# Optimization experiments

Hardware: AMD Instinct MI355X
Metric: run time of the kernel (lower is better)

Reference implementation:

```python
import jax, jax.numpy as jnp
import numpy as np
import math

B, S, D = 4, 2048, 1024
H, DH = 16, 64  # num_heads, head dim (hardcoded 64 in module)


def setup_inputs() -> dict:
    key = jax.random.key(0)
    ks = jax.random.split(key, 5)
    scale = 0.02
    return {
        "x": jax.random.normal(ks[0], (B, S, D), dtype=jnp.float32),
        "W_Q": jax.random.normal(ks[1], (D, H * DH), dtype=jnp.float32) * scale,
        "W_K": jax.random.normal(ks[2], (D, H * DH), dtype=jnp.float32) * scale,
        "W_V": jax.random.normal(ks[3], (D, H * DH), dtype=jnp.float32) * scale,
        "W_O": jax.random.normal(ks[4], (H * DH, D), dtype=jnp.float32) * scale,
        "ln_gamma": jnp.ones((D,), dtype=jnp.float32),
        "ln_beta": jnp.zeros((D,), dtype=jnp.float32),
    }


def reference(x, W_Q, W_K, W_V, W_O, ln_gamma, ln_beta):
    # QKV projections (bias=False Linear: x @ W)
    q = (x @ W_Q).reshape(B, S, H, DH).transpose(0, 2, 1, 3)  # [B,H,S,DH]
    k = (x @ W_K).reshape(B, S, H, DH).transpose(0, 2, 1, 3)
    v = (x @ W_V).reshape(B, S, H, DH).transpose(0, 2, 1, 3)

    # scaled scores with causal mask (upper triangle, diag=1 -> -1e7)
    scores = jnp.einsum("bhsd,bhtd->bhst", q, k) / math.sqrt(DH)  # [B,H,S,S]
    causal = jnp.triu(jnp.ones((S, S), dtype=bool), k=1)
    scores = jnp.where(causal, jnp.float32(-1e7), scores)
    attn = jax.nn.softmax(scores, axis=-1)
    ctx = jnp.einsum("bhst,bhtd->bhsd", attn, v)  # [B,H,S,DH]

    # merge heads, output proj, residual, LayerNorm
    out = ctx.transpose(0, 2, 1, 3).reshape(B, S, H * DH) @ W_O + x
    mu = jnp.mean(out, axis=-1, keepdims=True)
    var = jnp.mean((out - mu) ** 2, axis=-1, keepdims=True)
    out = (out - mu) * jax.lax.rsqrt(var + 1e-5) * ln_gamma + ln_beta
    return out
```

## Files before the change

### kernel.cpp

```cpp
#include <hip/hip_runtime.h>
#include <hip/hip_bf16.h>
#include <cstdint>
#include <cstddef>

#define S_ 2048
#define D_ 1024
#define H_ 16
#define DH_ 64
#define M_ 8192

using bf16 = __bf16;
using bf16x4 = __attribute__((ext_vector_type(4))) __bf16;
using bf16x8 = __attribute__((ext_vector_type(8))) __bf16;
using f32x4 = __attribute__((ext_vector_type(4))) float;
using s16x4 = __attribute__((ext_vector_type(4))) short;

__device__ __forceinline__ void g2lds16(const bf16* g, bf16* l) {
  __builtin_amdgcn_global_load_lds(
      (const __attribute__((address_space(1))) void*)g,
      (__attribute__((address_space(3))) void*)l, 16, 0, 0);
}

__device__ __forceinline__ f32x4 mfma16(bf16x4 a, bf16x4 b, f32x4 c) {
#if __has_builtin(__builtin_amdgcn_mfma_f32_16x16x16_bf16)
  return __builtin_amdgcn_mfma_f32_16x16x16_bf16(a, b, c, 0, 0, 0);
#elif __has_builtin(__builtin_amdgcn_mfma_f32_16x16x16bf16_1k)
  return __builtin_amdgcn_mfma_f32_16x16x16bf16_1k(
      __builtin_bit_cast(s16x4, a), __builtin_bit_cast(s16x4, b), c, 0, 0, 0);
#else
  f32x4 d;
  asm("v_mfma_f32_16x16x16_bf16 %0, %1, %2, %3"
      : "=v"(d)
      : "v"(a), "v"(b), "v"(c));
  return d;
#endif
}

__global__ __launch_bounds__(256) void cvt_all_kernel(
    const float* __restrict__ x, const float* __restrict__ w0,
    const float* __restrict__ w1, const float* __restrict__ w2,
    const float* __restrict__ w3, bf16* __restrict__ xb,
    bf16* __restrict__ o0, bf16* __restrict__ o1, bf16* __restrict__ o2,
    bf16* __restrict__ o3) {
  __shared__ float tile[32][33];
  int bx = blockIdx.x;
  int tid = threadIdx.x;
  if (bx < 4096) {
    size_t i = ((size_t)bx * 256 + tid) * 8;
    float4 a = *(const float4*)(x + i);
    float4 b = *(const float4*)(x + i + 4);
    bf16x8 o;
    o[0] = (bf16)a.x; o[1] = (bf16)a.y; o[2] = (bf16)a.z; o[3] = (bf16)a.w;
    o[4] = (bf16)b.x; o[5] = (bf16)b.y; o[6] = (bf16)b.z; o[7] = (bf16)b.w;
    *(bf16x8*)(xb + i) = o;
    return;
  }
  int wb = bx - 4096;
  int wsel = wb >> 10; wb &= 1023;
  const float* W; bf16* O;
  switch (wsel) {
    case 0: W = w0; O = o0; break;
    case 1: W = w1; O = o1; break;
    case 2: W = w2; O = o2; break;
    default: W = w3; O = o3; break;
  }
  int n0 = (wb & 31) * 32;
  int k0 = (wb >> 5) * 32;
#pragma unroll
  for (int i = 0; i < 4; ++i) {
    int e = tid + i * 256; int rr = e >> 5, cc = e & 31;
    tile[rr][cc] = W[(size_t)(k0 + rr) * 1024 + n0 + cc];
  }
  __syncthreads();
#pragma unroll
  for (int i = 0; i < 4; ++i) {
    int e = tid + i * 256; int rr = e >> 5, cc = e & 31;
    O[(size_t)(n0 + rr) * 1024 + k0 + cc] = (bf16)tile[cc][rr];
  }
}

template <int MODE>
__global__ __launch_bounds__(256) void gemm_kernel(
    const bf16* __restrict__ A,
    const bf16* __restrict__ Bt0, const bf16* __restrict__ Bt1,
    const bf16* __restrict__ Bt2,
    bf16* __restrict__ Qo, bf16* __restrict__ Ko, bf16* __restrict__ Vto,
    const float* __restrict__ xres, float* __restrict__ out) {
  __shared__ __align__(16) bf16 smA[128 * 32];
  __shared__ __align__(16) bf16 smB[128 * 32];
  constexpr int NBLK = (MODE == 0) ? 24 : 8;
  int bm = blockIdx.x / NBLK, bn = blockIdx.x % NBLK;
  int m0 = bm * 128;
  const bf16* Bt; int which = 0, n0;
  if constexpr (MODE == 0) {
    which = bn >> 3; n0 = (bn & 7) * 128;
    Bt = (which == 0) ? Bt0 : (which == 1 ? Bt1 : Bt2);
  } else { n0 = bn * 128; Bt = Bt0; }

  int tid = threadIdx.x;
  int wave = tid >> 6, lane = tid & 63;
  int quad = lane >> 4, r = lane & 15;
  int wm = (wave >> 1) * 64, wn = (wave & 1) * 64;

  f32x4 acc[4][4];
  f32x4 zero = {0.f, 0.f, 0.f, 0.f};
#pragma unroll
  for (int i = 0; i < 4; ++i)
#pragma unroll
    for (int j = 0; j < 4; ++j) acc[i][j] = zero;

  int c0 = 2 * wave, c1 = 2 * wave + 1;
  int rA0 = c0 * 16 + (lane >> 2);
  int rA1 = c1 * 16 + (lane >> 2);
  int kc = (lane & 3) * 8;

  for (int k0 = 0; k0 < 1024; k0 += 32) {
    __syncthreads();
    const bf16 *gA0, *gA1;
    if constexpr (MODE == 0) {
      gA0 = A + (size_t)(m0 + rA0) * 1024 + k0 + kc;
      gA1 = A + (size_t)(m0 + rA1) * 1024 + k0 + kc;
    } else {
      int kk = k0 + kc, h = kk >> 6, dh = kk & 63;
      int mm0 = m0 + rA0, mm1 = m0 + rA1;
      gA0 = A + ((size_t)((mm0 >> 11) * H_ + h) * S_ + (mm0 & 2047)) * DH_ + dh;
      gA1 = A + ((size_t)((mm1 >> 11) * H_ + h) * S_ + (mm1 & 2047)) * DH_ + dh;
    }
    g2lds16(gA0, smA + c0 * 512);
    g2lds16(gA1, smA + c1 * 512);
    g2lds16(Bt + (size_t)(n0 + rA0) * 1024 + k0 + kc, smB + c0 * 512);
    g2lds16(Bt + (size_t)(n0 + rA1) * 1024 + k0 + kc, smB + c1 * 512);
    __syncthreads();
    bf16x8 af[4], bfr[4];
#pragma unroll
    for (int i = 0; i < 4; ++i)
      af[i] = *(const bf16x8*)(smA + (wm + i * 16 + r) * 32 + quad * 8);
#pragma unroll
    for (int j = 0; j < 4; ++j)
      bfr[j] = *(const bf16x8*)(smB + (wn + j * 16 + r) * 32 + quad * 8);
    if (which == 2) {
#pragma unroll
      for (int i = 0; i < 4; ++i)
#pragma unroll
        for (int j = 0; j < 4; ++j)
          acc[i][j] = __builtin_amdgcn_mfma_f32_16x16x32_bf16(bfr[i], af[j],
                                                              acc[i][j], 0, 0, 0);
    } else {
#pragma unroll
      for (int i = 0; i < 4; ++i)
#pragma unroll
        for (int j = 0; j < 4; ++j)
          acc[i][j] = __builtin_amdgcn_mfma_f32_16x16x32_bf16(af[i], bfr[j],
                                                              acc[i][j], 0, 0, 0);
    }
  }

  if (which == 2) {
#pragma unroll
    for (int i = 0; i < 4; ++i) {
#pragma unroll
      for (int j = 0; j < 4; ++j) {
#pragma unroll
        for (int g = 0; g < 4; ++g) {
          int n = n0 + wn + i * 16 + quad * 4 + g;
          int m = m0 + wm + j * 16 + r;
          Vto[((size_t)((m >> 11) * H_ + (n >> 6)) * DH_ + (n & 63)) * S_ +
              (m & 2047)] = (bf16)acc[i][j][g];
        }
      }
    }
    return;
  }
#pragma unroll
  for (int i = 0; i < 4; ++i) {
#pragma unroll
    for (int j = 0; j < 4; ++j) {
#pragma unroll
      for (int g = 0; g < 4; ++g) {
        int m = m0 + wm + i * 16 + quad * 4 + g;
        int n = n0 + wn + j * 16 + r;
        float v = acc[i][j][g];
        if constexpr (MODE == 0) {
          int b = m >> 11, s = m & 2047, h = n >> 6, dh = n & 63;
          if (which == 0)
            Qo[((size_t)(b * H_ + h) * S_ + s) * DH_ + dh] = (bf16)v;
          else
            Ko[((size_t)(b * H_ + h) * S_ + s) * DH_ + dh] = (bf16)v;
        } else {
          size_t idx = (size_t)m * 1024 + n;
          out[idx] = v + xres[idx];
        }
      }
    }
  }
}

__global__ __launch_bounds__(256) void attn_kernel(const bf16* __restrict__ Qb,
                                                   const bf16* __restrict__ Kb,
                                                   const bf16* __restrict__ Vtb,
                                                   bf16* __restrict__ ctx) {
  __shared__ __align__(16) bf16 smK[2][64 * 64];
  __shared__ __align__(16) bf16 smV[2][64 * 64];
  const int bh = blockIdx.x & 63, p = blockIdx.x >> 6;
  const bf16* Qh = Qb + (size_t)bh * S_ * DH_;
  const bf16* Kh = Kb + (size_t)bh * S_ * DH_;
  const bf16* Vh = Vtb + (size_t)bh * DH_ * S_;
  bf16* Ch = ctx + (size_t)bh * S_ * DH_;
  const int tid = threadIdx.x, wave = tid >> 6, lane = tid & 63;
  const int quad = lane >> 4, r = lane & 15;
  const int r7 = r & 7;
  const int c0 = 2 * wave, c1 = c0 + 1;
  const int sr = lane >> 3;
  const int gcol = ((lane & 7) ^ (sr & 7)) * 8;
  const f32x4 zero = {0.f, 0.f, 0.f, 0.f};
  const int xk0 = (quad ^ r7) * 8, xk1 = ((quad + 4) ^ r7) * 8;

  for (int ph = 0; ph < 2; ++ph) {
    const int i128 = ph ? (15 - p) : p;
    const int qB = i128 * 128;
    const int q0w = qB + wave * 32;
    const int numkt = 2 * i128 + 2;

    bf16x8 qf[2][2];
    const float qsc = 0.125f * 1.44269504f;
#pragma unroll
    for (int qg = 0; qg < 2; ++qg)
#pragma unroll
      for (int hh = 0; hh < 2; ++hh) {
        bf16x8 q = *(const bf16x8*)(Qh + (size_t)(q0w + qg * 16 + r) * DH_ +
                                    hh * 32 + quad * 8);
#pragma unroll
        for (int i = 0; i < 8; ++i) q[i] = (bf16)((float)q[i] * qsc);
        qf[qg][hh] = q;
      }

    f32x4 lacc[2] = {zero, zero};
    f32x4 oacc[2][4];
#pragma unroll
    for (int qg = 0; qg < 2; ++qg)
#pragma unroll
      for (int tn = 0; tn < 4; ++tn) oacc[qg][tn] = zero;

    g2lds16(Kh + (size_t)(c0 * 8 + sr) * DH_ + gcol, &smK[0][c0 * 512]);
    g2lds16(Kh + (size_t)(c1 * 8 + sr) * DH_ + gcol, &smK[0][c1 * 512]);
    g2lds16(Vh + (size_t)(c0 * 8 + sr) * S_ + gcol, &smV[0][c0 * 512]);
    g2lds16(Vh + (size_t)(c1 * 8 + sr) * S_ + gcol, &smV[0][c1 * 512]);

    for (int kt = 0; kt < numkt; ++kt) {
      const int cur = kt & 1;
      const int kv0 = kt * 64;
      if (kt + 1 < numkt) {
        const int nk = kv0 + 64;
        g2lds16(Kh + (size_t)(nk + c0 * 8 + sr) * DH_ + gcol, &smK[1 - cur][c0 * 512]);
        g2lds16(Kh + (size_t)(nk + c1 * 8 + sr) * DH_ + gcol, &smK[1 - cur][c1 * 512]);
        g2lds16(Vh + (size_t)(c0 * 8 + sr) * S_ + nk + gcol, &smV[1 - cur][c0 * 512]);
        g2lds16(Vh + (size_t)(c1 * 8 + sr) * S_ + nk + gcol, &smV[1 - cur][c1 * 512]);
        asm volatile("s_waitcnt vmcnt(4)\n\ts_barrier" ::: "memory");
      } else {
        asm volatile("s_waitcnt vmcnt(0)\n\ts_barrier" ::: "memory");
      }
      if (kv0 <= q0w + 31) {
        const bf16* kb = &smK[cur][0];
        const bf16* vb = &smV[cur][0];

        f32x4 s[2][4];
#pragma unroll
        for (int t = 0; t < 4; ++t) {
          bf16x8 kf0 = *(const bf16x8*)(kb + (t * 16 + r) * 64 + xk0);
          bf16x8 kf1 = *(const bf16x8*)(kb + (t * 16 + r) * 64 + xk1);
#pragma unroll
          for (int qg = 0; qg < 2; ++qg) {
            f32x4 z = __builtin_amdgcn_mfma_f32_16x16x32_bf16(kf0, qf[qg][0],
                                                              zero, 0, 0, 0);
            s[qg][t] = __builtin_amdgcn_mfma_f32_16x16x32_bf16(kf1, qf[qg][1],
                                                               z, 0, 0, 0);
          }
        }
        if (kt >= numkt - 2) {
#pragma unroll
          for (int qg = 0; qg < 2; ++qg) {
            const int q = q0w + qg * 16 + r;
#pragma unroll
            for (int t = 0; t < 4; ++t) {
              const int kv = kv0 + t * 16 + quad * 4;
#pragma unroll
              for (int g = 0; g < 4; ++g)
                if (kv + g > q) s[qg][t][g] = -1e30f;
            }
          }
        }
#pragma unroll
        for (int t = 0; t < 4; ++t) {
          bf16x4 pa[2];
#pragma unroll
          for (int qg = 0; qg < 2; ++qg) {
#pragma unroll
            for (int g = 0; g < 4; ++g)
              s[qg][t][g] = __builtin_amdgcn_exp2f(s[qg][t][g]);
            lacc[qg] += s[qg][t];
            bf16x4 pk;
#pragma unroll
            for (int g = 0; g < 4; ++g) pk[g] = (bf16)s[qg][t][g];
            pa[qg] = pk;
          }
#pragma unroll
          for (int tn = 0; tn < 4; ++tn) {
            bf16x4 vf = *(const bf16x4*)(
                vb + (tn * 16 + r) * 64 +
                ((2 * t + (quad >> 1)) ^ r7) * 8 + (quad & 1) * 4);
            oacc[0][tn] = mfma16(pa[0], vf, oacc[0][tn]);
            oacc[1][tn] = mfma16(pa[1], vf, oacc[1][tn]);
          }
        }
      }
      asm volatile("s_waitcnt lgkmcnt(0)\n\ts_barrier" ::: "memory");
    }

#pragma unroll
    for (int qg = 0; qg < 2; ++qg) {
      float rs = (lacc[qg][0] + lacc[qg][1]) + (lacc[qg][2] + lacc[qg][3]);
      rs += __shfl_xor(rs, 16, 64);
      rs += __shfl_xor(rs, 32, 64);
      const float inv = 1.f / rs;
      f32x4 ib;
#pragma unroll
      for (int g = 0; g < 4; ++g) ib[g] = __shfl(inv, quad * 4 + g, 64);
#pragma unroll
      for (int tn = 0; tn < 4; ++tn) {
        f32x4 ov = oacc[qg][tn] * ib;
#pragma unroll
        for (int g = 0; g < 4; ++g)
          Ch[(size_t)(q0w + qg * 16 + quad * 4 + g) * DH_ + tn * 16 + r] =
              (bf16)ov[g];
      }
    }
  }
}

__global__ __launch_bounds__(256) void ln_kernel(float* __restrict__ out,
                                                 const float* __restrict__ gamma,
                                                 const float* __restrict__ beta) {
  __shared__ float red[8];
  size_t row = blockIdx.x;
  float* p = out + row * 1024;
  int tid = threadIdx.x;
  float4 v = ((const float4*)p)[tid];
  float s1 = v.x + v.y + v.z + v.w;
  float s2 = v.x * v.x + v.y * v.y + v.z * v.z + v.w * v.w;
#pragma unroll
  for (int o = 1; o < 64; o <<= 1) {
    s1 += __shfl_xor(s1, o, 64);
    s2 += __shfl_xor(s2, o, 64);
  }
  int wave = tid >> 6, lane = tid & 63;
  if (lane == 0) { red[wave] = s1; red[4 + wave] = s2; }
  __syncthreads();
  s1 = red[0] + red[1] + red[2] + red[3];
  s2 = red[4] + red[5] + red[6] + red[7];
  float mean = s1 * (1.f / 1024.f);
  float var = s2 * (1.f / 1024.f) - mean * mean;
  float rstd = rsqrtf(var + 1e-5f);
  float4 g = ((const float4*)gamma)[tid];
  float4 b = ((const float4*)beta)[tid];
  float4 o;
  o.x = (v.x - mean) * rstd * g.x + b.x;
  o.y = (v.y - mean) * rstd * g.y + b.y;
  o.z = (v.z - mean) * rstd * g.z + b.z;
  o.w = (v.w - mean) * rstd * g.w + b.w;
  ((float4*)p)[tid] = o;
}

extern "C" void kernel_launch(void* const* d_in, const int* in_sizes, int n_in,
                              void* d_out, int out_size, void* d_ws,
                              size_t ws_size, hipStream_t stream) {
  (void)in_sizes; (void)n_in; (void)out_size; (void)ws_size;
  const float* x  = (const float*)d_in[0];
  const float* WQ = (const float*)d_in[1];
  const float* WK = (const float*)d_in[2];
  const float* WV = (const float*)d_in[3];
  const float* WO = (const float*)d_in[4];
  const float* gamma = (const float*)d_in[5];
  const float* beta  = (const float*)d_in[6];
  float* out = (float*)d_out;

  bf16* ws = (bf16*)d_ws;
  const size_t MD = (size_t)M_ * D_;
  const size_t WW = (size_t)D_ * D_;
  bf16* xb   = ws;
  bf16* wqt  = xb + MD;
  bf16* wkt  = wqt + WW;
  bf16* wvt  = wkt + WW;
  bf16* wot  = wvt + WW;
  bf16* Qb   = wot + WW;
  bf16* Kb   = Qb + MD;
  bf16* Vtb  = Kb + MD;
  bf16* ctxb = Vtb + MD;

  cvt_all_kernel<<<dim3(8192), dim3(256), 0, stream>>>(
      x, WQ, WK, WV, WO, xb, wqt, wkt, wvt, wot);
  gemm_kernel<0><<<dim3(64 * 24), dim3(256), 0, stream>>>(
      xb, wqt, wkt, wvt, Qb, Kb, Vtb, nullptr, nullptr);
  attn_kernel<<<dim3(512), dim3(256), 0, stream>>>(Qb, Kb, Vtb, ctxb);
  gemm_kernel<1><<<dim3(64 * 8), dim3(256), 0, stream>>>(
      ctxb, wot, nullptr, nullptr, nullptr, nullptr, nullptr, x, out);
  ln_kernel<<<dim3(8192), dim3(256), 0, stream>>>(out, gamma, beta);
}
```

Baseline: 279.8 us.

## Double-buffer GEMM LDS tiles and XOR-swizzle k-chunks to avoid bank conflicts

The projection GEMM kernel now keeps two LDS buffers for A and B. The next k-tile is fetched with global_load_lds while the current one is used for MFMA, and explicit vmcnt waits plus barriers replace the two __syncthreads per iteration. The k-chunk column each lane writes and reads is also XOR-swizzled by row bits to reduce LDS bank conflicts. This doubles the LDS footprint and depends on the inline-asm waitcnt counts being correct for overlap to be safe.

```diff
diff --git a/kernel.cpp b/kernel.cpp
--- a/kernel.cpp
+++ b/kernel.cpp
@@ -86,8 +86,8 @@
     const bf16* __restrict__ Bt2,
     bf16* __restrict__ Qo, bf16* __restrict__ Ko, bf16* __restrict__ Vto,
     const float* __restrict__ xres, float* __restrict__ out) {
-  __shared__ __align__(16) bf16 smA[128 * 32];
-  __shared__ __align__(16) bf16 smB[128 * 32];
+  __shared__ __align__(16) bf16 smA[2][128 * 32];
+  __shared__ __align__(16) bf16 smB[2][128 * 32];
   constexpr int NBLK = (MODE == 0) ? 24 : 8;
   int bm = blockIdx.x / NBLK, bn = blockIdx.x % NBLK;
   int m0 = bm * 128;
@@ -112,32 +112,45 @@
   int c0 = 2 * wave, c1 = 2 * wave + 1;
   int rA0 = c0 * 16 + (lane >> 2);
   int rA1 = c1 * 16 + (lane >> 2);
-  int kc = (lane & 3) * 8;
-
-  for (int k0 = 0; k0 < 1024; k0 += 32) {
-    __syncthreads();
+  int kc = (((lane & 3) ^ ((lane >> 3) & 3)) * 8);
+  const int rx = ((r >> 1) & 3);
+
+  auto stage = [&](int k0, bf16* bufA, bf16* bufB) {
     const bf16 *gA0, *gA1;
     if constexpr (MODE == 0) {
       gA0 = A + (size_t)(m0 + rA0) * 1024 + k0 + kc;
       gA1 = A + (size_t)(m0 + rA1) * 1024 + k0 + kc;
     } else {
-      int kk = k0 + kc, h = kk >> 6, dh = kk & 63;
+      int kk0 = k0 + kc, h = kk0 >> 6, dh = kk0 & 63;
       int mm0 = m0 + rA0, mm1 = m0 + rA1;
       gA0 = A + ((size_t)((mm0 >> 11) * H_ + h) * S_ + (mm0 & 2047)) * DH_ + dh;
       gA1 = A + ((size_t)((mm1 >> 11) * H_ + h) * S_ + (mm1 & 2047)) * DH_ + dh;
     }
-    g2lds16(gA0, smA + c0 * 512);
-    g2lds16(gA1, smA + c1 * 512);
-    g2lds16(Bt + (size_t)(n0 + rA0) * 1024 + k0 + kc, smB + c0 * 512);
-    g2lds16(Bt + (size_t)(n0 + rA1) * 1024 + k0 + kc, smB + c1 * 512);
-    __syncthreads();
+    g2lds16(gA0, bufA + c0 * 512);
+    g2lds16(gA1, bufA + c1 * 512);
+    g2lds16(Bt + (size_t)(n0 + rA0) * 1024 + k0 + kc, bufB + c0 * 512);
+    g2lds16(Bt + (size_t)(n0 + rA1) * 1024 + k0 + kc, bufB + c1 * 512);
+  };
+
+  stage(0, &smA[0][0], &smB[0][0]);
+
+  for (int kt = 0; kt < 32; ++kt) {
+    const int cur = kt & 1;
+    if (kt + 1 < 32) {
+      stage((kt + 1) * 32, &smA[1 - cur][0], &smB[1 - cur][0]);
+      asm volatile("s_waitcnt vmcnt(4)\n\ts_barrier" ::: "memory");
+    } else {
+      asm volatile("s_waitcnt vmcnt(0)\n\ts_barrier" ::: "memory");
+    }
     bf16x8 af[4], bfr[4];
 #pragma unroll
     for (int i = 0; i < 4; ++i)
-      af[i] = *(const bf16x8*)(smA + (wm + i * 16 + r) * 32 + quad * 8);
+      af[i] = *(const bf16x8*)(&smA[cur][0] + (wm + i * 16 + r) * 32 +
+                               (quad ^ rx) * 8);
 #pragma unroll
     for (int j = 0; j < 4; ++j)
-      bfr[j] = *(const bf16x8*)(smB + (wn + j * 16 + r) * 32 + quad * 8);
+      bfr[j] = *(const bf16x8*)(&smB[cur][0] + (wn + j * 16 + r) * 32 +
+                                (quad ^ rx) * 8);
     if (which == 2) {
 #pragma unroll
       for (int i = 0; i < 4; ++i)
@@ -153,6 +166,7 @@
           acc[i][j] = __builtin_amdgcn_mfma_f32_16x16x32_bf16(af[i], bfr[j],
                                                               acc[i][j], 0, 0, 0);
     }
+    asm volatile("s_waitcnt lgkmcnt(0)\n\ts_barrier" ::: "memory");
   }
 
   if (which == 2) {
```

Result: slower. 293.9 us (+5.0%).
